# Kernel tuning notes

Measured on AMD Instinct MI355X. Metric: run time of the kernel, lower is better.

## Reference

```python
import jax, jax.numpy as jnp
import numpy as np

NEG_INF = -1e30

def setup_inputs() -> dict:
    key = jax.random.key(0)
    k1, k2, k3, k4, k5 = jax.random.split(key, 5)
    B, N, Fin, Fout, H = 8, 1024, 128, 64, 4
    h = jax.random.normal(k1, (B, N, Fin), dtype=jnp.float32)
    adj = jax.random.randint(k2, (N, N), 0, 2, dtype=jnp.int32)
    bias_matrix = jax.random.normal(k3, (1, 1, N, N), dtype=jnp.float32)
    # xavier-ish scaled params
    W = jax.random.normal(k4, (H, Fin, Fout), dtype=jnp.float32) * (1.0 / np.sqrt(Fin))
    a = jax.random.normal(k5, (H, 2 * Fout, 1), dtype=jnp.float32) * (1.0 / np.sqrt(2 * Fout))
    return {"h": h, "adj": adj, "bias_matrix": bias_matrix, "W": W, "a": a}


def reference(h, adj, bias_matrix, W, a):
    B, N, _ = h.shape
    H, _, Fout = W.shape
    # h_prime: [B, N, H, Fout]
    h_prime = jnp.einsum('bni,hio->bnho', h, W)
    # split attention vector: a_input @ a == h_i @ a1 + h_j @ a2 (same math, no O(N^2*F) tensor)
    a1 = a[:, :Fout, 0]   # [H, Fout]
    a2 = a[:, Fout:, 0]   # [H, Fout]
    ei = jnp.einsum('bnhf,hf->bnh', h_prime, a1)  # [B, N, H]
    ej = jnp.einsum('bnhf,hf->bnh', h_prime, a2)  # [B, N, H]
    e = jax.nn.leaky_relu(ei[:, :, None, :] + ej[:, None, :, :], negative_slope=0.2)  # [B,N,N,H]
    # bias_matrix [1,1,N,N] -> expand to [B,1,N,N] -> permute(0,2,3,1) -> [B,N,N,1]
    bias = jnp.transpose(bias_matrix, (0, 2, 3, 1))  # [1, N, N, 1], broadcasts to [B,N,N,H]
    e = e + bias
    mask = (adj != 0)[None, :, :, None]  # [1, N, N, 1]
    e_masked = jnp.where(mask, e, NEG_INF)
    attention = jax.nn.softmax(e_masked, axis=2)  # softmax over j
    h_out = jnp.einsum('bijh,bjhf->bihf', attention, h_prime)  # [B, N, H, Fout]
    return h_out.reshape(B, N, H * Fout)
```

## Files before the change

### kernel.cpp

```cpp
#include <hip/hip_runtime.h>

constexpr int B = 8, N = 1024, FIN = 128, FOUT = 64, H = 4;
constexpr float LOG2E = 1.44269504f;

typedef __attribute__((ext_vector_type(8))) short short8;
typedef __attribute__((ext_vector_type(4))) short short4v;
typedef __attribute__((ext_vector_type(4))) float f32x4;

static __device__ inline unsigned short f2bf(float x) {
    union { float f; unsigned u; } v; v.f = x;
    unsigned r = v.u + 0x7fff + ((v.u >> 16) & 1);
    return (unsigned short)(r >> 16);
}

__global__ __launch_bounds__(256) void gat_prep(
    const float* __restrict__ h,
    const float* __restrict__ W,
    const float* __restrict__ a,
    const int*   __restrict__ adj,
    const float* __restrict__ bias,
    unsigned short* __restrict__ hpF,
    float* __restrict__ mbF,
    float* __restrict__ ei_t,
    float* __restrict__ ej_t)
{
    __shared__ float h_lds[8][132];
    const int t = threadIdx.x;

    if (blockIdx.x < 512) {
        const int bx   = blockIdx.x;
        const int ti   = bx >> 3;
        const int jc   = (bx & 7) * 4 + (t >> 6);
        const int lane = t & 63;
        const int i    = ti * 16 + (lane & 15);
        const int j0   = jc * 32 + 8 * (lane >> 4);

        const int4*   ap = reinterpret_cast<const int4*>(adj + (size_t)i * N + j0);
        const float4* bp = reinterpret_cast<const float4*>(bias + (size_t)i * N + j0);
        int4   a0 = ap[0], a1 = ap[1];
        float4 b0 = bp[0], b1 = bp[1];
        float4 o0, o1;
        o0.x = a0.x ? LOG2E * b0.x : -1e35f;
        o0.y = a0.y ? LOG2E * b0.y : -1e35f;
        o0.z = a0.z ? LOG2E * b0.z : -1e35f;
        o0.w = a0.w ? LOG2E * b0.w : -1e35f;
        o1.x = a1.x ? LOG2E * b1.x : -1e35f;
        o1.y = a1.y ? LOG2E * b1.y : -1e35f;
        o1.z = a1.z ? LOG2E * b1.z : -1e35f;
        o1.w = a1.w ? LOG2E * b1.w : -1e35f;

        float* dst = mbF + (((size_t)ti * 32 + jc) * 64 + lane) * 8;
        *reinterpret_cast<float4*>(dst)     = o0;
        *reinterpret_cast<float4*>(dst + 4) = o1;
        return;
    }

    const int blk = blockIdx.x - 512;
    const int b   = blk >> 7;
    const int n0  = (blk & 127) * 8;

    {
        const float* src = h + ((size_t)b * N + n0) * FIN;
        float4 x = reinterpret_cast<const float4*>(src)[t];
        int fl = t * 4;
        *reinterpret_cast<float4*>(&h_lds[fl >> 7][fl & 127]) = x;
    }
    __syncthreads();

    const int hd   = t >> 6;
    const int lane = t & 63;
    const int li   = lane & 15;
    const int f0   = li * 4;
    const int g    = (lane >> 4) & 1;
    const int kh   = lane >> 5;

    float acc[4][4];
    #pragma unroll
    for (int k = 0; k < 4; ++k)
        #pragma unroll
        for (int j = 0; j < 4; ++j) acc[k][j] = 0.f;

    const float* Wp = W + (size_t)hd * FIN * FOUT + (size_t)kh * 64 * FOUT + f0;
    #pragma unroll 4
    for (int i = 0; i < 64; ++i) {
        float4 w4 = *reinterpret_cast<const float4*>(Wp + (size_t)i * FOUT);
        #pragma unroll
        for (int k = 0; k < 4; ++k) {
            float hv = h_lds[4 * g + k][kh * 64 + i];
            acc[k][0] = fmaf(hv, w4.x, acc[k][0]);
            acc[k][1] = fmaf(hv, w4.y, acc[k][1]);
            acc[k][2] = fmaf(hv, w4.z, acc[k][2]);
            acc[k][3] = fmaf(hv, w4.w, acc[k][3]);
        }
    }

    #pragma unroll
    for (int k = 0; k < 4; ++k)
        #pragma unroll
        for (int j = 0; j < 4; ++j)
            acc[k][j] += __shfl_xor(acc[k][j], 32, 64);

    const int bh = b * H + hd;
    if (kh == 0) {
        const int jc  = n0 >> 5;
        const int kgp = (n0 >> 3) & 3;
        const int ft  = li >> 2;
        const int e0  = 4 * g;
        #pragma unroll
        for (int jj = 0; jj < 4; ++jj) {
            short4v v4;
            v4[0] = (short)f2bf(acc[0][jj]);
            v4[1] = (short)f2bf(acc[1][jj]);
            v4[2] = (short)f2bf(acc[2][jj]);
            v4[3] = (short)f2bf(acc[3][jj]);
            const int lanep = (4 * (li & 3) + jj) + 16 * kgp;
            *reinterpret_cast<short4v*>(
                hpF + ((((size_t)bh * 32 + jc) * 4 + ft) * 64 + lanep) * 8 + e0) = v4;
        }
    }

    float4 a1 = *reinterpret_cast<const float4*>(a + (size_t)hd * 2 * FOUT + f0);
    float4 a2 = *reinterpret_cast<const float4*>(a + (size_t)hd * 2 * FOUT + FOUT + f0);
    #pragma unroll
    for (int k = 0; k < 4; ++k) {
        float e1 = acc[k][0] * a1.x + acc[k][1] * a1.y + acc[k][2] * a1.z + acc[k][3] * a1.w;
        float e2 = acc[k][0] * a2.x + acc[k][1] * a2.y + acc[k][2] * a2.z + acc[k][3] * a2.w;
        #pragma unroll
        for (int m = 1; m < 16; m <<= 1) {
            e1 += __shfl_xor(e1, m, 64);
            e2 += __shfl_xor(e2, m, 64);
        }
        if ((lane & 15) == 0 && kh == 0) {
            int r = n0 + 4 * g + k;
            ei_t[(size_t)bh * N + r] = LOG2E * e1;
            ej_t[(size_t)bh * N + r] = LOG2E * e2;
        }
    }
}

__global__ __launch_bounds__(512) void gat_attn(
    const unsigned short* __restrict__ hpF,
    const float* __restrict__ ei_t,
    const float* __restrict__ ej_t,
    const float* __restrict__ mbF,
    float* __restrict__ out)
{
    __shared__ f32x4 red[5][4][64];
    const int raw  = blockIdx.x;
    const int xcd  = raw & 7;
    const int k_   = raw >> 3;
    const int bh   = ((xcd >> 1) << 3) | (k_ >> 3);
    const int it0  = (((xcd & 1) << 3) | (k_ & 7)) * 4;
    const int t    = threadIdx.x;
    const int w8   = t >> 6;
    const int w    = w8 & 3;
    const int jh   = w8 >> 2;
    const int lane = t & 63;
    const int li   = lane & 15;
    const int kg   = lane >> 4;
    const int ti   = it0 + w;
    const int irow = ti * 16 + li;
    const int jcb  = jh * 16;

    const float  ei0   = ei_t[(size_t)bh * N + irow];
    const float* ejrow = ej_t + (size_t)bh * N;
    const float* mrow  = mbF + ((size_t)ti * 32 * 64 + lane) * 8;
    const unsigned short* hrow = hpF + ((size_t)bh * 32 * 4 * 64 + lane) * 8;

    f32x4 c0 = {0.f,0.f,0.f,0.f}, c1 = {0.f,0.f,0.f,0.f};
    f32x4 c2 = {0.f,0.f,0.f,0.f}, c3 = {0.f,0.f,0.f,0.f};
    f32x4 c4 = {0.f,0.f,0.f,0.f};
    const short obf = (short)0x3F80;
    const short8 ones = {obf,obf,obf,obf,obf,obf,obf,obf};

    #define DECLS(S) float4 ejA##S, ejB##S, mA##S, mB##S; \
                     short8 bA##S, bB##S, bC##S, bD##S;
    #define LOADS(S, JC) {                                                   \
        ejA##S = *reinterpret_cast<const float4*>(ejrow + (JC) * 32 + 8 * kg);\
        ejB##S = *reinterpret_cast<const float4*>(ejrow + (JC) * 32 + 8 * kg + 4);\
        mA##S  = *reinterpret_cast<const float4*>(mrow + (JC) * 512);        \
        mB##S  = *reinterpret_cast<const float4*>(mrow + (JC) * 512 + 4);    \
        bA##S  = *reinterpret_cast<const short8*>(hrow + (JC) * 2048);       \
        bB##S  = *reinterpret_cast<const short8*>(hrow + (JC) * 2048 + 512); \
        bC##S  = *reinterpret_cast<const short8*>(hrow + (JC) * 2048 + 1024);\
        bD##S  = *reinterpret_cast<const short8*>(hrow + (JC) * 2048 + 1536); }
    #define SCORE(PD, EJ, MBV) {                                             \
        float e_ = ei0 + (EJ);                                               \
        e_ = fmaxf(e_, 0.2f * e_) + (MBV);                                   \
        asm("v_exp_f32 %0, %1" : "=v"(PD) : "v"(e_)); }
    #define COMPS(S) {                                                       \
        float p0,p1,p2,p3,p4,p5,p6,p7;                                       \
        SCORE(p0, ejA##S.x, mA##S.x) SCORE(p1, ejA##S.y, mA##S.y)            \
        SCORE(p2, ejA##S.z, mA##S.z) SCORE(p3, ejA##S.w, mA##S.w)            \
        SCORE(p4, ejB##S.x, mB##S.x) SCORE(p5, ejB##S.y, mB##S.y)            \
        SCORE(p6, ejB##S.z, mB##S.z) SCORE(p7, ejB##S.w, mB##S.w)            \
        int4 pk_;                                                            \
        asm("v_cvt_pk_bf16_f32 %0, %1, %2" : "=v"(pk_.x) : "v"(p0), "v"(p1));\
        asm("v_cvt_pk_bf16_f32 %0, %1, %2" : "=v"(pk_.y) : "v"(p2), "v"(p3));\
        asm("v_cvt_pk_bf16_f32 %0, %1, %2" : "=v"(pk_.z) : "v"(p4), "v"(p5));\
        asm("v_cvt_pk_bf16_f32 %0, %1, %2" : "=v"(pk_.w) : "v"(p6), "v"(p7));\
        short8 a0_ = *reinterpret_cast<short8*>(&pk_);                       \
        c0 = __builtin_amdgcn_mfma_f32_16x16x32_bf16(a0_, bA##S, c0, 0,0,0); \
        c1 = __builtin_amdgcn_mfma_f32_16x16x32_bf16(a0_, bB##S, c1, 0,0,0); \
        c2 = __builtin_amdgcn_mfma_f32_16x16x32_bf16(a0_, bC##S, c2, 0,0,0); \
        c3 = __builtin_amdgcn_mfma_f32_16x16x32_bf16(a0_, bD##S, c3, 0,0,0); \
        c4 = __builtin_amdgcn_mfma_f32_16x16x32_bf16(a0_, ones,  c4, 0,0,0); }

    DECLS(0) DECLS(1)
    LOADS(0, jcb)
    #pragma unroll 2
    for (int jc = 0; jc < 16; jc += 2) {
        LOADS(1, jcb + jc + 1)
        COMPS(0)
        if (jc + 2 < 16) LOADS(0, jcb + jc + 2)
        COMPS(1)
    }
    #undef DECLS
    #undef LOADS
    #undef SCORE
    #undef COMPS

    if (jh == 1) {
        red[0][w][lane] = c0;
        red[1][w][lane] = c1;
        red[2][w][lane] = c2;
        red[3][w][lane] = c3;
        red[4][w][lane] = c4;
    }
    __syncthreads();
    if (jh == 1) return;

    c0 += red[0][w][lane];
    c1 += red[1][w][lane];
    c2 += red[2][w][lane];
    c3 += red[3][w][lane];
    c4 += red[4][w][lane];

    const int b  = bh >> 2;
    const int hd = bh & 3;
    #pragma unroll
    for (int r = 0; r < 4; ++r) {
        int orow = ti * 16 + 4 * kg + r;
        float inv = 1.0f / c4[r];
        float* ob = out + (((size_t)b * N + orow) * H + hd) * 64 + li;
        ob[0]  = c0[r] * inv;
        ob[16] = c1[r] * inv;
        ob[32] = c2[r] * inv;
        ob[48] = c3[r] * inv;
    }
}

extern "C" void kernel_launch(void* const* d_in, const int* in_sizes, int n_in,
                              void* d_out, int out_size, void* d_ws, size_t ws_size,
                              hipStream_t stream) {
    const float* h    = (const float*)d_in[0];
    const int*   adj  = (const int*)  d_in[1];
    const float* bias = (const float*)d_in[2];
    const float* W    = (const float*)d_in[3];
    const float* a    = (const float*)d_in[4];
    float* out = (float*)d_out;

    char* ws = (char*)d_ws;
    unsigned short* hpF = (unsigned short*)ws;
    float* mbF  = (float*)(ws + (size_t)B * H * 64 * N * 2);
    float* ei_t = (float*)(ws + (size_t)B * H * 64 * N * 2 + (size_t)N * N * 4);
    float* ej_t = ei_t + (size_t)B * H * N;

    gat_prep<<<512 + B * N / 8, 256, 0, stream>>>(h, W, a, adj, bias,
                                                  hpF, mbF, ei_t, ej_t);
    gat_attn<<<B * H * (N / 64), 512, 0, stream>>>(hpF, ei_t, ej_t, mbF, out);
}
```

Before: 42.57 us.

## Store mask-bias as bf16 and stage h_prime tiles through LDS with async loads

```diff
diff --git a/kernel.cpp b/kernel.cpp
--- a/kernel.cpp
+++ b/kernel.cpp
@@ -20,7 +20,7 @@
     const int*   __restrict__ adj,
     const float* __restrict__ bias,
     unsigned short* __restrict__ hpF,
-    float* __restrict__ mbF,
+    unsigned short* __restrict__ mbB,
     float* __restrict__ ei_t,
     float* __restrict__ ej_t)
 {
@@ -39,19 +39,20 @@
         const float4* bp = reinterpret_cast<const float4*>(bias + (size_t)i * N + j0);
         int4   a0 = ap[0], a1 = ap[1];
         float4 b0 = bp[0], b1 = bp[1];
-        float4 o0, o1;
-        o0.x = a0.x ? LOG2E * b0.x : -1e35f;
-        o0.y = a0.y ? LOG2E * b0.y : -1e35f;
-        o0.z = a0.z ? LOG2E * b0.z : -1e35f;
-        o0.w = a0.w ? LOG2E * b0.w : -1e35f;
-        o1.x = a1.x ? LOG2E * b1.x : -1e35f;
-        o1.y = a1.y ? LOG2E * b1.y : -1e35f;
-        o1.z = a1.z ? LOG2E * b1.z : -1e35f;
-        o1.w = a1.w ? LOG2E * b1.w : -1e35f;
-
-        float* dst = mbF + (((size_t)ti * 32 + jc) * 64 + lane) * 8;
-        *reinterpret_cast<float4*>(dst)     = o0;
-        *reinterpret_cast<float4*>(dst + 4) = o1;
+        unsigned short q0 = f2bf(a0.x ? LOG2E * b0.x : -1e35f);
+        unsigned short q1 = f2bf(a0.y ? LOG2E * b0.y : -1e35f);
+        unsigned short q2 = f2bf(a0.z ? LOG2E * b0.z : -1e35f);
+        unsigned short q3 = f2bf(a0.w ? LOG2E * b0.w : -1e35f);
+        unsigned short q4 = f2bf(a1.x ? LOG2E * b1.x : -1e35f);
+        unsigned short q5 = f2bf(a1.y ? LOG2E * b1.y : -1e35f);
+        unsigned short q6 = f2bf(a1.z ? LOG2E * b1.z : -1e35f);
+        unsigned short q7 = f2bf(a1.w ? LOG2E * b1.w : -1e35f);
+        int4 ov;
+        ov.x = (int)((unsigned)q0 | ((unsigned)q1 << 16));
+        ov.y = (int)((unsigned)q2 | ((unsigned)q3 << 16));
+        ov.z = (int)((unsigned)q4 | ((unsigned)q5 << 16));
+        ov.w = (int)((unsigned)q6 | ((unsigned)q7 << 16));
+        *reinterpret_cast<int4*>(mbB + (((size_t)ti * 32 + jc) * 64 + lane) * 8) = ov;
         return;
     }
 
@@ -142,9 +143,10 @@
     const unsigned short* __restrict__ hpF,
     const float* __restrict__ ei_t,
     const float* __restrict__ ej_t,
-    const float* __restrict__ mbF,
+    const unsigned short* __restrict__ mbB,
     float* __restrict__ out)
 {
+    __shared__ __align__(16) unsigned short hstage[2][2][4][512];
     __shared__ f32x4 red[5][4][64];
     const int raw  = blockIdx.x;
     const int xcd  = raw & 7;
@@ -164,8 +166,8 @@
 
     const float  ei0   = ei_t[(size_t)bh * N + irow];
     const float* ejrow = ej_t + (size_t)bh * N;
-    const float* mrow  = mbF + ((size_t)ti * 32 * 64 + lane) * 8;
-    const unsigned short* hrow = hpF + ((size_t)bh * 32 * 4 * 64 + lane) * 8;
+    const unsigned short* mrow = mbB + ((size_t)ti * 32 * 64 + lane) * 8;
+    const size_t hbase = (size_t)bh * 65536;
 
     f32x4 c0 = {0.f,0.f,0.f,0.f}, c1 = {0.f,0.f,0.f,0.f};
     f32x4 c2 = {0.f,0.f,0.f,0.f}, c3 = {0.f,0.f,0.f,0.f};
@@ -173,51 +175,72 @@
     const short obf = (short)0x3F80;
     const short8 ones = {obf,obf,obf,obf,obf,obf,obf,obf};
 
-    #define DECLS(S) float4 ejA##S, ejB##S, mA##S, mB##S; \
-                     short8 bA##S, bB##S, bC##S, bD##S;
-    #define LOADS(S, JC) {                                                   \
-        ejA##S = *reinterpret_cast<const float4*>(ejrow + (JC) * 32 + 8 * kg);\
-        ejB##S = *reinterpret_cast<const float4*>(ejrow + (JC) * 32 + 8 * kg + 4);\
-        mA##S  = *reinterpret_cast<const float4*>(mrow + (JC) * 512);        \
-        mB##S  = *reinterpret_cast<const float4*>(mrow + (JC) * 512 + 4);    \
-        bA##S  = *reinterpret_cast<const short8*>(hrow + (JC) * 2048);       \
-        bB##S  = *reinterpret_cast<const short8*>(hrow + (JC) * 2048 + 512); \
-        bC##S  = *reinterpret_cast<const short8*>(hrow + (JC) * 2048 + 1024);\
-        bD##S  = *reinterpret_cast<const short8*>(hrow + (JC) * 2048 + 1536); }
-    #define SCORE(PD, EJ, MBV) {                                             \
-        float e_ = ei0 + (EJ);                                               \
-        e_ = fmaxf(e_, 0.2f * e_) + (MBV);                                   \
-        asm("v_exp_f32 %0, %1" : "=v"(PD) : "v"(e_)); }
-    #define COMPS(S) {                                                       \
-        float p0,p1,p2,p3,p4,p5,p6,p7;                                       \
-        SCORE(p0, ejA##S.x, mA##S.x) SCORE(p1, ejA##S.y, mA##S.y)            \
-        SCORE(p2, ejA##S.z, mA##S.z) SCORE(p3, ejA##S.w, mA##S.w)            \
-        SCORE(p4, ejB##S.x, mB##S.x) SCORE(p5, ejB##S.y, mB##S.y)            \
-        SCORE(p6, ejB##S.z, mB##S.z) SCORE(p7, ejB##S.w, mB##S.w)            \
-        int4 pk_;                                                            \
-        asm("v_cvt_pk_bf16_f32 %0, %1, %2" : "=v"(pk_.x) : "v"(p0), "v"(p1));\
-        asm("v_cvt_pk_bf16_f32 %0, %1, %2" : "=v"(pk_.y) : "v"(p2), "v"(p3));\
-        asm("v_cvt_pk_bf16_f32 %0, %1, %2" : "=v"(pk_.z) : "v"(p4), "v"(p5));\
-        asm("v_cvt_pk_bf16_f32 %0, %1, %2" : "=v"(pk_.w) : "v"(p6), "v"(p7));\
-        short8 a0_ = *reinterpret_cast<short8*>(&pk_);                       \
-        c0 = __builtin_amdgcn_mfma_f32_16x16x32_bf16(a0_, bA##S, c0, 0,0,0); \
-        c1 = __builtin_amdgcn_mfma_f32_16x16x32_bf16(a0_, bB##S, c1, 0,0,0); \
-        c2 = __builtin_amdgcn_mfma_f32_16x16x32_bf16(a0_, bC##S, c2, 0,0,0); \
-        c3 = __builtin_amdgcn_mfma_f32_16x16x32_bf16(a0_, bD##S, c3, 0,0,0); \
-        c4 = __builtin_amdgcn_mfma_f32_16x16x32_bf16(a0_, ones,  c4, 0,0,0); }
-
-    DECLS(0) DECLS(1)
-    LOADS(0, jcb)
-    #pragma unroll 2
+    #define STAGE(BUF, JCG) {                                                 \
+        const unsigned short* gs_ = hpF + hbase + (size_t)(JCG) * 2048        \
+                                        + (size_t)w * 512 + (size_t)lane * 8; \
+        __builtin_amdgcn_global_load_lds(                                     \
+            (const __attribute__((address_space(1))) void*)gs_,               \
+            (__attribute__((address_space(3))) void*)&hstage[BUF][jh][w][0],  \
+            16, 0, 0); }
+
+    #define DSREAD(BUF, BA, BB, BC, BD) {                                     \
+        BA = *reinterpret_cast<const short8*>(&hstage[BUF][jh][0][lane * 8]); \
+        BB = *reinterpret_cast<const short8*>(&hstage[BUF][jh][1][lane * 8]); \
+        BC = *reinterpret_cast<const short8*>(&hstage[BUF][jh][2][lane * 8]); \
+        BD = *reinterpret_cast<const short8*>(&hstage[BUF][jh][3][lane * 8]); }
+
+    #define SCORE2(PL, PH, EJL, EJH, QW) {                                    \
+        float bl_ = __uint_as_float(((unsigned)(QW)) << 16);                  \
+        float bh_ = __uint_as_float(((unsigned)(QW)) & 0xffff0000u);          \
+        float el_ = ei0 + (EJL); el_ = fmaxf(el_, 0.2f * el_) + bl_;          \
+        float eh_ = ei0 + (EJH); eh_ = fmaxf(eh_, 0.2f * eh_) + bh_;          \
+        asm("v_exp_f32 %0, %1" : "=v"(PL) : "v"(el_));                        \
+        asm("v_exp_f32 %0, %1" : "=v"(PH) : "v"(eh_)); }
+
+    #define COMPS(MQ, BA, BB, BC, BD, JC) {                                   \
+        float4 ejA = *reinterpret_cast<const float4*>(ejrow + (JC) * 32 + 8 * kg);     \
+        float4 ejB = *reinterpret_cast<const float4*>(ejrow + (JC) * 32 + 8 * kg + 4); \
+        float p0,p1,p2,p3,p4,p5,p6,p7;                                        \
+        SCORE2(p0, p1, ejA.x, ejA.y, MQ.x)                                    \
+        SCORE2(p2, p3, ejA.z, ejA.w, MQ.y)                                    \
+        SCORE2(p4, p5, ejB.x, ejB.y, MQ.z)                                    \
+        SCORE2(p6, p7, ejB.z, ejB.w, MQ.w)                                    \
+        int4 pk_;                                                             \
+        asm("v_cvt_pk_bf16_f32 %0, %1, %2" : "=v"(pk_.x) : "v"(p0), "v"(p1)); \
+        asm("v_cvt_pk_bf16_f32 %0, %1, %2" : "=v"(pk_.y) : "v"(p2), "v"(p3)); \
+        asm("v_cvt_pk_bf16_f32 %0, %1, %2" : "=v"(pk_.z) : "v"(p4), "v"(p5)); \
+        asm("v_cvt_pk_bf16_f32 %0, %1, %2" : "=v"(pk_.w) : "v"(p6), "v"(p7)); \
+        short8 a0_ = *reinterpret_cast<short8*>(&pk_);                        \
+        c0 = __builtin_amdgcn_mfma_f32_16x16x32_bf16(a0_, BA, c0, 0, 0, 0);   \
+        c1 = __builtin_amdgcn_mfma_f32_16x16x32_bf16(a0_, BB, c1, 0, 0, 0);   \
+        c2 = __builtin_amdgcn_mfma_f32_16x16x32_bf16(a0_, BC, c2, 0, 0, 0);   \
+        c3 = __builtin_amdgcn_mfma_f32_16x16x32_bf16(a0_, BD, c3, 0, 0, 0);   \
+        c4 = __builtin_amdgcn_mfma_f32_16x16x32_bf16(a0_, ones, c4, 0, 0, 0); }
+
+    short8 A0, B0, C0, D0, A1, B1, C1, D1;
+    int4 mq0, mq1;
+
+    STAGE(0, jcb)
+    mq0 = *reinterpret_cast<const int4*>(mrow + (size_t)jcb * 512);
+    __syncthreads();
+
     for (int jc = 0; jc < 16; jc += 2) {
-        LOADS(1, jcb + jc + 1)
-        COMPS(0)
-        if (jc + 2 < 16) LOADS(0, jcb + jc + 2)
-        COMPS(1)
-    }
-    #undef DECLS
-    #undef LOADS
-    #undef SCORE
+        STAGE(1, jcb + jc + 1)
+        mq1 = *reinterpret_cast<const int4*>(mrow + (size_t)(jcb + jc + 1) * 512);
+        DSREAD(0, A0, B0, C0, D0)
+        COMPS(mq0, A0, B0, C0, D0, jcb + jc)
+        __syncthreads();
+        if (jc + 2 < 16) {
+            STAGE(0, jcb + jc + 2)
+            mq0 = *reinterpret_cast<const int4*>(mrow + (size_t)(jcb + jc + 2) * 512);
+        }
+        DSREAD(1, A1, B1, C1, D1)
+        COMPS(mq1, A1, B1, C1, D1, jcb + jc + 1)
+        __syncthreads();
+    }
+    #undef STAGE
+    #undef DSREAD
+    #undef SCORE2
     #undef COMPS
 
     if (jh == 1) {
@@ -262,11 +285,11 @@
 
     char* ws = (char*)d_ws;
     unsigned short* hpF = (unsigned short*)ws;
-    float* mbF  = (float*)(ws + (size_t)B * H * 64 * N * 2);
-    float* ei_t = (float*)(ws + (size_t)B * H * 64 * N * 2 + (size_t)N * N * 4);
+    unsigned short* mbB = (unsigned short*)(ws + ((size_t)4 << 20));
+    float* ei_t = (float*)(ws + ((size_t)6 << 20));
     float* ej_t = ei_t + (size_t)B * H * N;
 
     gat_prep<<<512 + B * N / 8, 256, 0, stream>>>(h, W, a, adj, bias,
-                                                  hpF, mbF, ei_t, ej_t);
-    gat_attn<<<B * H * (N / 64), 512, 0, stream>>>(hpF, ei_t, ej_t, mbF, out);
-}
+                                                  hpF, mbB, ei_t, ej_t);
+    gat_attn<<<B * H * (N / 64), 512, 0, stream>>>(hpF, ei_t, ej_t, mbB, out);
+}
```

New measurement: 38.11 us. -10.5%, faster.
